# Kernel optimization log

Measured on AMD Instinct MI355X. Metric: run time of the kernel, lower is better.

The kernel has to match this reference:

```python
import jax, jax.numpy as jnp
import numpy as np

OBS, HID, H, A = 128, 256, 512, 16
T, B = 256, 256


def setup_inputs() -> dict:
    key = jax.random.key(0)
    ks = jax.random.split(key, 8)
    s = lambda k, shape, fan_in: jax.random.normal(k, shape, jnp.float32) / np.sqrt(fan_in).astype(np.float32)
    return {
        "x": jax.random.normal(ks[0], (T, B, OBS), jnp.float32),
        "W_enc": s(ks[1], (OBS, HID), OBS),
        "b_enc": jnp.zeros((HID,), jnp.float32),
        "Wi": s(ks[2], (HID, 4 * H), HID),      # input->gates kernel (i,f,g,o)
        "Wh": s(ks[3], (H, 4 * H), H),          # hidden->gates kernel
        "b_lstm": jnp.zeros((4 * H,), jnp.float32),
        "W_mu": s(ks[4], (H, A), H),
        "b_mu": jnp.zeros((A,), jnp.float32),
        "log_std": jnp.zeros((1, A), jnp.float32),
        "W_v": s(ks[5], (H, 1), H),
        "b_v": jnp.zeros((1,), jnp.float32),
    }


def reference(x, W_enc, b_enc, Wi, Wh, b_lstm, W_mu, b_mu, log_std, W_v, b_v):
    # Encoder MLP: Linear + gelu, mapping obs_dim -> hidden_features.
    feats = jax.nn.gelu(x @ W_enc + b_enc)            # (T, B, HID)
    # Precompute the input contribution to all 4 gates for every timestep
    # (same math as flax OptimizedLSTMCell, hoisted out of the scan).
    x_gates = feats @ Wi + b_lstm                      # (T, B, 4H)
    bsz = x.shape[1]
    c0 = jnp.zeros((bsz, H), x.dtype)
    h0 = jnp.zeros((bsz, H), x.dtype)

    def step(carry, xg):
        c, h = carry
        z = xg + h @ Wh                                # (B, 4H)
        i, f, g, o = jnp.split(z, 4, axis=-1)          # flax gate order i,f,g,o
        c_new = jax.nn.sigmoid(f) * c + jax.nn.sigmoid(i) * jnp.tanh(g)
        h_new = jax.nn.sigmoid(o) * jnp.tanh(c_new)
        return (c_new, h_new), h_new

    _, hs = jax.lax.scan(step, (c0, h0), x_gates)      # hs: (T, B, H)
    # Heads (dropout is identity in eval/deterministic mode).
    mu = hs @ W_mu + b_mu                              # (T, B, A)
    sigma = jnp.broadcast_to(jnp.exp(log_std), mu.shape)
    value = hs @ W_v + b_v                             # (T, B, 1)
    return mu, sigma, value
```

## Files before the change

kernel.cpp:

```cpp
#include <hip/hip_runtime.h>
#include <stdint.h>

#define T_STEPS 256
#define BATCH   256
#define OBS     128
#define HID     256
#define HSZ     512
#define NG      16
#define RPG     16
#define NSLICES 16
#define HCS     32
#define GCOLS   128
#define RING_SLOT_W 65536

typedef __attribute__((ext_vector_type(8))) short short8;
typedef __attribute__((ext_vector_type(4))) float f32x4;
typedef __attribute__((ext_vector_type(4))) int   i32x4;

__device__ __forceinline__ unsigned short f2bf(float x) {
    union { float f; uint32_t u; } v; v.f = x;
    uint32_t r = v.u + 0x7FFF + ((v.u >> 16) & 1);
    return (unsigned short)(r >> 16);
}
__device__ __forceinline__ float sigmoidf_(float x) { return 1.f / (1.f + __expf(-x)); }
__device__ __forceinline__ float tanhf_(float x)    { return 1.f - 2.f / (1.f + __expf(2.f * x)); }

#define GLD4(d0, d1, d2, d3, p, O0, O1, O2, O3)                                 \
    asm volatile("global_load_dwordx4 %0, %4, off offset:" #O0 " sc0 sc1\n\t"   \
                 "global_load_dwordx4 %1, %4, off offset:" #O1 " sc0 sc1\n\t"   \
                 "global_load_dwordx4 %2, %4, off offset:" #O2 " sc0 sc1\n\t"   \
                 "global_load_dwordx4 %3, %4, off offset:" #O3 " sc0 sc1"       \
                 : "=&v"(d0), "=&v"(d1), "=&v"(d2), "=&v"(d3) : "v"(p))

__global__ __launch_bounds__(256) void enc_kernel(
    const float* __restrict__ x, const float* __restrict__ W_enc,
    const float* __restrict__ b_enc, unsigned short* __restrict__ feats) {
    __shared__ unsigned short wlds[HID * OBS];
    int tid = threadIdx.x;
    for (int idx = tid; idx < OBS * HID; idx += 256) {
        int k = idx >> 8, n = idx & 255;
        int byte = ((n * OBS + k) * 2) ^ ((n & 7) << 4);
        *(unsigned short*)((char*)wlds + byte) = f2bf(W_enc[k * HID + n]);
    }
    __syncthreads();
    int wave = tid >> 6, lane = tid & 63;
    long m0 = (long)blockIdx.x * 64 + wave * 16;
    int arow = lane & 15, kq = lane >> 4;
    f32x4 acc[16];
    f32x4 z4 = {0.f, 0.f, 0.f, 0.f};
#pragma unroll
    for (int i = 0; i < 16; i++) acc[i] = z4;
#pragma unroll
    for (int kk = 0; kk < OBS; kk += 32) {
        const float* ap = x + (m0 + arow) * OBS + kk + kq * 8;
        float4 a0 = *(const float4*)ap;
        float4 a1 = *(const float4*)(ap + 4);
        short8 af;
        af[0] = (short)f2bf(a0.x); af[1] = (short)f2bf(a0.y);
        af[2] = (short)f2bf(a0.z); af[3] = (short)f2bf(a0.w);
        af[4] = (short)f2bf(a1.x); af[5] = (short)f2bf(a1.y);
        af[6] = (short)f2bf(a1.z); af[7] = (short)f2bf(a1.w);
#pragma unroll
        for (int nt = 0; nt < 16; nt++) {
            int n = nt * 16 + arow;
            int byte = ((n * OBS + kk + kq * 8) * 2) ^ ((n & 7) << 4);
            short8 bf = *(const short8*)((char*)wlds + byte);
            acc[nt] = __builtin_amdgcn_mfma_f32_16x16x32_bf16(af, bf, acc[nt], 0, 0, 0);
        }
    }
#pragma unroll
    for (int nt = 0; nt < 16; nt++) {
        int col = nt * 16 + (lane & 15);
        float bias = b_enc[col];
#pragma unroll
        for (int j = 0; j < 4; j++) {
            long row = m0 + kq * 4 + j;
            float z = acc[nt][j] + bias;
            float zc = 0.79788456f * (z + 0.044715f * z * z * z);
            float g = 0.5f * z * (1.f + tanhf_(zc));
            feats[row * HID + col] = f2bf(g);
        }
    }
}

__global__ __launch_bounds__(256) void prep_wi(
    const float* __restrict__ Wi, unsigned short* __restrict__ Wipk) {
    int t = blockIdx.x * 256 + threadIdx.x;
    int f = t & 15, l = (t >> 4) & 63, w = (t >> 10) & 3, s = t >> 12;
    int ct = f >> 3, i = f & 7;
    int n = w * 32 + ct * 16 + (l & 15);
    int colg = (n & 3) * HSZ + s * HCS + (n >> 2);
    int kbase = i * 32 + (l >> 4) * 8;
    short8 v;
#pragma unroll
    for (int j = 0; j < 8; j++) v[j] = (short)f2bf(Wi[(kbase + j) * 2048 + colg]);
    *(short8*)(Wipk + (long)t * 8) = v;
}

__device__ __forceinline__ void spin_flags(const uint32_t* fl, int lane) {
    const uint32_t* p = fl + (lane & 15);
    while (true) {
        uint32_t got = (lane < 16)
            ? __hip_atomic_load(p, __ATOMIC_RELAXED, __HIP_MEMORY_SCOPE_AGENT) : 1u;
        if (__all(got != 0)) break;
    }
}

__global__ __launch_bounds__(256) void scan_kernel(
    const float* __restrict__ Wh, const float* __restrict__ b_lstm,
    const unsigned short* __restrict__ feats, const unsigned short* __restrict__ Wipk,
    uint32_t* __restrict__ ring, uint32_t* __restrict__ flags,
    uint32_t* __restrict__ hs32) {
    __shared__ unsigned short whs[GCOLS * HSZ];
    __shared__ unsigned short hst[RPG * HSZ];
    __shared__ float zt[RPG][132];
    const int tid = threadIdx.x;
    const int g = blockIdx.x & 15;
    const int slice = blockIdx.x >> 4;
    const int rowg = g * RPG;

    for (int idx = tid; idx < GCOLS * HSZ; idx += 256) {
        int n = idx & 127, k = idx >> 7;
        int colg = (n & 3) * HSZ + slice * HCS + (n >> 2);
        int byte = ((n * HSZ + k) * 2) ^ ((n & 7) << 4);
        *(unsigned short*)((char*)whs + byte) = f2bf(Wh[k * 2048 + colg]);
    }
    const int wave = tid >> 6, lane = tid & 63;
    const int wc = wave * 32;
    const int arow = lane & 15, kq = lane >> 4;
    const int n0 = wc + arow, n1 = wc + 16 + arow;
    short8 wif0[8], wif1[8];
    {
        const short8* wp = (const short8*)Wipk + ((slice * 4 + wave) * 64 + lane) * 16;
#pragma unroll
        for (int i = 0; i < 8; i++) { wif0[i] = wp[i]; wif1[i] = wp[8 + i]; }
    }
    const int grow = tid >> 4, hp = tid & 15;
    float bl0[4], bl1[4];
#pragma unroll
    for (int q = 0; q < 4; q++) {
        bl0[q] = b_lstm[q * HSZ + slice * HCS + 2 * hp];
        bl1[q] = b_lstm[q * HSZ + slice * HCS + 2 * hp + 1];
    }
    float c0 = 0.f, c1 = 0.f;
    const int srow = tid >> 4, sc64 = tid & 15;
    const int sw = (srow & 7) << 4;
    f32x4 z4 = {0.f, 0.f, 0.f, 0.f};
    __syncthreads();

    for (int t = 0; t < T_STEPS; ++t) {
        f32x4 acc0 = z4, acc1 = z4;
        const char* fb = (const char*)feats + ((long)t * BATCH + rowg + arow) * (HID * 2) + kq * 16;
#pragma unroll
        for (int i = 0; i < 8; i++) {
            short8 af = *(const short8*)(fb + i * 64);
            acc0 = __builtin_amdgcn_mfma_f32_16x16x32_bf16(af, wif0[i], acc0, 0, 0, 0);
            acc1 = __builtin_amdgcn_mfma_f32_16x16x32_bf16(af, wif1[i], acc1, 0, 0, 0);
        }
        __builtin_amdgcn_sched_barrier(0);
        if (t > 0) {
            if (tid < 64) spin_flags(flags + ((long)g * T_STEPS + t - 1) * 16, lane);
            __syncthreads();
            const char* hb = (const char*)ring + ((t - 1) & 3) * (RING_SLOT_W * 4)
                           + (rowg + srow) * 1024 + sc64 * 64;
            i32x4 S0, S1, S2, S3;
            GLD4(S0, S1, S2, S3, hb, 0, 16, 32, 48);
            asm volatile("s_waitcnt vmcnt(0)" ::: "memory");
            __builtin_amdgcn_sched_barrier(0);
            int sb = srow * 1024 + sc64 * 64;
            *(i32x4*)((char*)hst + ((sb +  0) ^ sw)) = S0;
            *(i32x4*)((char*)hst + ((sb + 16) ^ sw)) = S1;
            *(i32x4*)((char*)hst + ((sb + 32) ^ sw)) = S2;
            *(i32x4*)((char*)hst + ((sb + 48) ^ sw)) = S3;
            __syncthreads();
#pragma unroll
            for (int i = 0; i < 16; i++) {
                short8 ah = *(const short8*)((char*)hst
                              + ((arow * 1024 + i * 64 + kq * 16) ^ ((arow & 7) << 4)));
                int kk = i * 32 + kq * 8;
                short8 b0 = *(const short8*)((char*)whs + (((n0 * HSZ + kk) * 2) ^ ((n0 & 7) << 4)));
                short8 b1 = *(const short8*)((char*)whs + (((n1 * HSZ + kk) * 2) ^ ((n1 & 7) << 4)));
                acc0 = __builtin_amdgcn_mfma_f32_16x16x32_bf16(ah, b0, acc0, 0, 0, 0);
                acc1 = __builtin_amdgcn_mfma_f32_16x16x32_bf16(ah, b1, acc1, 0, 0, 0);
            }
        }
#pragma unroll
        for (int j = 0; j < 4; j++) {
            zt[kq * 4 + j][wc + arow]      = acc0[j];
            zt[kq * 4 + j][wc + 16 + arow] = acc1[j];
        }
        __syncthreads();
        float4 r0 = *(const float4*)&zt[grow][8 * hp];
        float4 r1 = *(const float4*)&zt[grow][8 * hp + 4];
        c0 = sigmoidf_(r0.y + bl0[1]) * c0 + sigmoidf_(r0.x + bl0[0]) * tanhf_(r0.z + bl0[2]);
        c1 = sigmoidf_(r1.y + bl1[1]) * c1 + sigmoidf_(r1.x + bl1[0]) * tanhf_(r1.z + bl1[2]);
        float h0 = sigmoidf_(r0.w + bl0[3]) * tanhf_(c0);
        float h1 = sigmoidf_(r1.w + bl1[3]) * tanhf_(c1);
        uint32_t wv = (uint32_t)f2bf(h0) | ((uint32_t)f2bf(h1) << 16);
        uint32_t* wp = ring + (t & 3) * RING_SLOT_W + (rowg + grow) * 256 + slice * 16 + hp;
        __hip_atomic_store(wp, wv, __ATOMIC_RELAXED, __HIP_MEMORY_SCOPE_AGENT);
        hs32[((long)t * BATCH + rowg + grow) * 256 + slice * 16 + hp] = wv;
        __syncthreads();
        if (tid == 0)
            __hip_atomic_store(flags + ((long)g * T_STEPS + t) * 16 + slice, 1u,
                               __ATOMIC_RELAXED, __HIP_MEMORY_SCOPE_AGENT);
    }
}

__global__ __launch_bounds__(256) void heads_kernel(
    const unsigned short* __restrict__ hs, const float* __restrict__ W_mu,
    const float* __restrict__ b_mu, const float* __restrict__ log_std,
    const float* __restrict__ W_v, const float* __restrict__ b_v,
    float* __restrict__ mu_out, float* __restrict__ sig_out,
    float* __restrict__ val_out) {
    __shared__ unsigned short wlds[32 * HSZ];
    int tid = threadIdx.x;
    for (int idx = tid; idx < 32 * HSZ; idx += 256) {
        int n = idx & 31, k = idx >> 5;
        float w = 0.f;
        if (n < 16) w = W_mu[k * 16 + n];
        else if (n == 16) w = W_v[k];
        int byte = ((n * HSZ + k) * 2) ^ ((n & 7) << 4);
        *(unsigned short*)((char*)wlds + byte) = f2bf(w);
    }
    __syncthreads();
    int wave = tid >> 6, lane = tid & 63;
    long m0 = (long)blockIdx.x * 64 + wave * 16;
    int arow = lane & 15, kq = lane >> 4;
    f32x4 acc0 = {0.f, 0.f, 0.f, 0.f}, acc1 = {0.f, 0.f, 0.f, 0.f};
    const unsigned short* hr = hs + (m0 + arow) * HSZ + kq * 8;
#pragma unroll
    for (int kk = 0; kk < HSZ; kk += 32) {
        short8 af = *(const short8*)(hr + kk);
        int n0 = arow;
        int b0 = ((n0 * HSZ + kk + kq * 8) * 2) ^ ((n0 & 7) << 4);
        short8 bf0 = *(const short8*)((char*)wlds + b0);
        acc0 = __builtin_amdgcn_mfma_f32_16x16x32_bf16(af, bf0, acc0, 0, 0, 0);
        int n1 = 16 + arow;
        int b1 = ((n1 * HSZ + kk + kq * 8) * 2) ^ ((n1 & 7) << 4);
        short8 bf1 = *(const short8*)((char*)wlds + b1);
        acc1 = __builtin_amdgcn_mfma_f32_16x16x32_bf16(af, bf1, acc1, 0, 0, 0);
    }
    int col = lane & 15;
    float bm = b_mu[col];
    float sg = __expf(log_std[col]);
#pragma unroll
    for (int j = 0; j < 4; j++) {
        long row = m0 + kq * 4 + j;
        mu_out[row * 16 + col]  = acc0[j] + bm;
        sig_out[row * 16 + col] = sg;
    }
    if (col == 0) {
        float bv = b_v[0];
#pragma unroll
        for (int j = 0; j < 4; j++) {
            long row = m0 + kq * 4 + j;
            val_out[row] = acc1[j] + bv;
        }
    }
}

extern "C" void kernel_launch(void* const* d_in, const int* in_sizes, int n_in,
                              void* d_out, int out_size, void* d_ws, size_t ws_size,
                              hipStream_t stream) {
    const float* x      = (const float*)d_in[0];
    const float* W_enc  = (const float*)d_in[1];
    const float* b_enc  = (const float*)d_in[2];
    const float* Wi     = (const float*)d_in[3];
    const float* Wh     = (const float*)d_in[4];
    const float* b_lstm = (const float*)d_in[5];
    const float* W_mu   = (const float*)d_in[6];
    const float* b_mu   = (const float*)d_in[7];
    const float* lstd   = (const float*)d_in[8];
    const float* W_v    = (const float*)d_in[9];
    const float* b_v    = (const float*)d_in[10];

    char* ws = (char*)d_ws;
    uint32_t*       flags = (uint32_t*)ws;
    uint32_t*       ring  = (uint32_t*)(ws + (512 << 10));
    unsigned short* Wipk  = (unsigned short*)(ws + (1536 << 10));
    unsigned short* feats = (unsigned short*)(ws + (3584 << 10));
    unsigned short* hs    = (unsigned short*)(ws + (3584 << 10) + 33554432);

    float* mu_out  = (float*)d_out;
    float* sig_out = mu_out + 1048576;
    float* val_out = mu_out + 2097152;

    hipMemsetAsync(flags, 0, NG * T_STEPS * NSLICES * sizeof(uint32_t), stream);
    prep_wi<<<dim3(256), dim3(256), 0, stream>>>(Wi, Wipk);
    enc_kernel<<<dim3(1024), dim3(256), 0, stream>>>(x, W_enc, b_enc, feats);
    scan_kernel<<<dim3(256), dim3(256), 0, stream>>>(Wh, b_lstm, feats, Wipk,
                                                     ring, flags, (uint32_t*)hs);
    heads_kernel<<<dim3(1024), dim3(256), 0, stream>>>(hs, W_mu, b_mu, lstd, W_v, b_v,
                                                       mu_out, sig_out, val_out);
}
```

Baseline: 1.020 ms.

## Replace flag-based step sync with sentinel-polled ring and register-resident gate reshuffle

Drops the per-step flag array and block-wide barriers. Consumers poll the h ring data directly until no 0xFFFFFFFF sentinel is left, and producers reset the slot from two steps back to the sentinel. Half of the Wh slice now lives in registers, prepacked by a new prep_wh kernel, while the other half stays in LDS. The hidden-state tile is double-buffered, the feats rows for the next step are prefetched, and the gate reshuffle uses lane shuffles in place of an LDS transpose. Together these remove two syncthreads and a flag round-trip per timestep from the serial critical path. The cost is higher register pressure and reliance on the sentinel never being a legitimate pair of bf16 values.

Result: slower. 1.451 ms (+42.2%).

```diff
diff --git a/kernel.cpp b/kernel.cpp
--- a/kernel.cpp
+++ b/kernel.cpp
@@ -10,7 +10,6 @@
 #define RPG     16
 #define NSLICES 16
 #define HCS     32
-#define GCOLS   128
 #define RING_SLOT_W 65536
 
 typedef __attribute__((ext_vector_type(8))) short short8;
@@ -97,113 +96,160 @@
     *(short8*)(Wipk + (long)t * 8) = v;
 }
 
-__device__ __forceinline__ void spin_flags(const uint32_t* fl, int lane) {
-    const uint32_t* p = fl + (lane & 15);
-    while (true) {
-        uint32_t got = (lane < 16)
-            ? __hip_atomic_load(p, __ATOMIC_RELAXED, __HIP_MEMORY_SCOPE_AGENT) : 1u;
-        if (__all(got != 0)) break;
-    }
-}
-
-__global__ __launch_bounds__(256) void scan_kernel(
-    const float* __restrict__ Wh, const float* __restrict__ b_lstm,
-    const unsigned short* __restrict__ feats, const unsigned short* __restrict__ Wipk,
-    uint32_t* __restrict__ ring, uint32_t* __restrict__ flags,
+__global__ __launch_bounds__(256) void prep_wh(
+    const float* __restrict__ Wh, unsigned short* __restrict__ Whpk) {
+    int t = blockIdx.x * 256 + threadIdx.x;
+    int l = t & 63, i = (t >> 6) & 15, w = (t >> 10) & 3, s = t >> 12;
+    int n = w * 32 + (l & 15);
+    int colg = (n & 3) * HSZ + s * HCS + (n >> 2);
+    int kbase = i * 32 + (l >> 4) * 8;
+    short8 v;
+#pragma unroll
+    for (int j = 0; j < 8; j++) v[j] = (short)f2bf(Wh[(kbase + j) * 2048 + colg]);
+    *(short8*)(Whpk + (long)t * 8) = v;
+}
+
+__global__ __launch_bounds__(256, 1) void scan_kernel(
+    const float* __restrict__ b_lstm, const unsigned short* __restrict__ feats,
+    const unsigned short* __restrict__ Wipk, const unsigned short* __restrict__ Whpk,
+    const float* __restrict__ Wh, uint32_t* __restrict__ ring,
     uint32_t* __restrict__ hs32) {
-    __shared__ unsigned short whs[GCOLS * HSZ];
-    __shared__ unsigned short hst[RPG * HSZ];
-    __shared__ float zt[RPG][132];
+    __shared__ unsigned short whs[64 * HSZ];
+    __shared__ unsigned short hst[2 * RPG * HSZ];
     const int tid = threadIdx.x;
     const int g = blockIdx.x & 15;
     const int slice = blockIdx.x >> 4;
     const int rowg = g * RPG;
-
-    for (int idx = tid; idx < GCOLS * HSZ; idx += 256) {
-        int n = idx & 127, k = idx >> 7;
-        int colg = (n & 3) * HSZ + slice * HCS + (n >> 2);
-        int byte = ((n * HSZ + k) * 2) ^ ((n & 7) << 4);
+    const int wave = tid >> 6, lane = tid & 63;
+    const int arow = lane & 15, kq = lane >> 4;
+
+    for (int idx = tid; idx < 64 * HSZ; idx += 256) {
+        int np = idx & 63, k = idx >> 6;
+        int n1 = (np >> 4) * 32 + 16 + (np & 15);
+        int colg = (n1 & 3) * HSZ + slice * HCS + (n1 >> 2);
+        int byte = ((np * HSZ + k) * 2) ^ ((np & 7) << 4);
         *(unsigned short*)((char*)whs + byte) = f2bf(Wh[k * 2048 + colg]);
     }
-    const int wave = tid >> 6, lane = tid & 63;
-    const int wc = wave * 32;
-    const int arow = lane & 15, kq = lane >> 4;
-    const int n0 = wc + arow, n1 = wc + 16 + arow;
-    short8 wif0[8], wif1[8];
+    short8 wif0[8], wif1[8], whb[16];
     {
         const short8* wp = (const short8*)Wipk + ((slice * 4 + wave) * 64 + lane) * 16;
 #pragma unroll
         for (int i = 0; i < 8; i++) { wif0[i] = wp[i]; wif1[i] = wp[8 + i]; }
-    }
-    const int grow = tid >> 4, hp = tid & 15;
+        const short8* hp8 = (const short8*)Whpk;
+#pragma unroll
+        for (int i = 0; i < 16; i++)
+            whb[i] = hp8[((slice * 4 + wave) * 16 + i) * 64 + lane];
+    }
+    const int a_ = arow >> 2;
+    const int hcol0 = slice * HCS + wave * 8 + a_;
     float bl0[4], bl1[4];
 #pragma unroll
     for (int q = 0; q < 4; q++) {
-        bl0[q] = b_lstm[q * HSZ + slice * HCS + 2 * hp];
-        bl1[q] = b_lstm[q * HSZ + slice * HCS + 2 * hp + 1];
-    }
+        bl0[q] = b_lstm[q * HSZ + hcol0];
+        bl1[q] = b_lstm[q * HSZ + hcol0 + 4];
+    }
+    const int row = kq * 4 + (arow & 3);
+    int colw = slice * 16 + wave * 4 + ((a_ & 1) ? 2 + (a_ >> 1) : (a_ >> 1));
     float c0 = 0.f, c1 = 0.f;
     const int srow = tid >> 4, sc64 = tid & 15;
     const int sw = (srow & 7) << 4;
+    short8 ff[8];
+    {
+        const char* fb = (const char*)feats + ((long)(rowg + arow)) * (HID * 2) + kq * 16;
+#pragma unroll
+        for (int i = 0; i < 8; i++) ff[i] = *(const short8*)(fb + i * 64);
+    }
     f32x4 z4 = {0.f, 0.f, 0.f, 0.f};
     __syncthreads();
 
     for (int t = 0; t < T_STEPS; ++t) {
         f32x4 acc0 = z4, acc1 = z4;
-        const char* fb = (const char*)feats + ((long)t * BATCH + rowg + arow) * (HID * 2) + kq * 16;
 #pragma unroll
         for (int i = 0; i < 8; i++) {
-            short8 af = *(const short8*)(fb + i * 64);
-            acc0 = __builtin_amdgcn_mfma_f32_16x16x32_bf16(af, wif0[i], acc0, 0, 0, 0);
-            acc1 = __builtin_amdgcn_mfma_f32_16x16x32_bf16(af, wif1[i], acc1, 0, 0, 0);
+            acc0 = __builtin_amdgcn_mfma_f32_16x16x32_bf16(ff[i], wif0[i], acc0, 0, 0, 0);
+            acc1 = __builtin_amdgcn_mfma_f32_16x16x32_bf16(ff[i], wif1[i], acc1, 0, 0, 0);
+        }
+        {
+            int tn = (t + 1 < T_STEPS) ? t + 1 : t;
+            const char* fb = (const char*)feats
+                           + ((long)tn * BATCH + rowg + arow) * (HID * 2) + kq * 16;
+#pragma unroll
+            for (int i = 0; i < 8; i++) ff[i] = *(const short8*)(fb + i * 64);
         }
         __builtin_amdgcn_sched_barrier(0);
         if (t > 0) {
-            if (tid < 64) spin_flags(flags + ((long)g * T_STEPS + t - 1) * 16, lane);
-            __syncthreads();
-            const char* hb = (const char*)ring + ((t - 1) & 3) * (RING_SLOT_W * 4)
+            const char* pb = (const char*)ring + ((t - 1) & 3) * (RING_SLOT_W * 4)
                            + (rowg + srow) * 1024 + sc64 * 64;
             i32x4 S0, S1, S2, S3;
-            GLD4(S0, S1, S2, S3, hb, 0, 16, 32, 48);
-            asm volatile("s_waitcnt vmcnt(0)" ::: "memory");
+            while (true) {
+                GLD4(S0, S1, S2, S3, pb, 0, 16, 32, 48);
+                asm volatile("s_waitcnt vmcnt(0)" ::: "memory");
+                bool ok = S0[0] != -1 && S0[1] != -1 && S0[2] != -1 && S0[3] != -1
+                       && S1[0] != -1 && S1[1] != -1 && S1[2] != -1 && S1[3] != -1
+                       && S2[0] != -1 && S2[1] != -1 && S2[2] != -1 && S2[3] != -1
+                       && S3[0] != -1 && S3[1] != -1 && S3[2] != -1 && S3[3] != -1;
+                if (ok) break;
+                __builtin_amdgcn_s_sleep(1);
+            }
             __builtin_amdgcn_sched_barrier(0);
+            char* hb = (char*)hst + (t & 1) * 16384;
             int sb = srow * 1024 + sc64 * 64;
-            *(i32x4*)((char*)hst + ((sb +  0) ^ sw)) = S0;
-            *(i32x4*)((char*)hst + ((sb + 16) ^ sw)) = S1;
-            *(i32x4*)((char*)hst + ((sb + 32) ^ sw)) = S2;
-            *(i32x4*)((char*)hst + ((sb + 48) ^ sw)) = S3;
-            __syncthreads();
+            *(i32x4*)(hb + ((sb +  0) ^ sw)) = S0;
+            *(i32x4*)(hb + ((sb + 16) ^ sw)) = S1;
+            *(i32x4*)(hb + ((sb + 32) ^ sw)) = S2;
+            *(i32x4*)(hb + ((sb + 48) ^ sw)) = S3;
+        }
+        __syncthreads();
+        if (t > 0) {
+            const char* hb = (const char*)hst + (t & 1) * 16384;
+            const int np = wave * 16 + arow;
 #pragma unroll
             for (int i = 0; i < 16; i++) {
-                short8 ah = *(const short8*)((char*)hst
+                short8 ah = *(const short8*)(hb
                               + ((arow * 1024 + i * 64 + kq * 16) ^ ((arow & 7) << 4)));
-                int kk = i * 32 + kq * 8;
-                short8 b0 = *(const short8*)((char*)whs + (((n0 * HSZ + kk) * 2) ^ ((n0 & 7) << 4)));
-                short8 b1 = *(const short8*)((char*)whs + (((n1 * HSZ + kk) * 2) ^ ((n1 & 7) << 4)));
-                acc0 = __builtin_amdgcn_mfma_f32_16x16x32_bf16(ah, b0, acc0, 0, 0, 0);
+                short8 b1 = *(const short8*)((char*)whs
+                              + ((np * 1024 + i * 64 + kq * 16) ^ ((np & 7) << 4)));
+                acc0 = __builtin_amdgcn_mfma_f32_16x16x32_bf16(ah, whb[i], acc0, 0, 0, 0);
                 acc1 = __builtin_amdgcn_mfma_f32_16x16x32_bf16(ah, b1, acc1, 0, 0, 0);
             }
         }
-#pragma unroll
-        for (int j = 0; j < 4; j++) {
-            zt[kq * 4 + j][wc + arow]      = acc0[j];
-            zt[kq * 4 + j][wc + 16 + arow] = acc1[j];
-        }
-        __syncthreads();
-        float4 r0 = *(const float4*)&zt[grow][8 * hp];
-        float4 r1 = *(const float4*)&zt[grow][8 * hp + 4];
-        c0 = sigmoidf_(r0.y + bl0[1]) * c0 + sigmoidf_(r0.x + bl0[0]) * tanhf_(r0.z + bl0[2]);
-        c1 = sigmoidf_(r1.y + bl1[1]) * c1 + sigmoidf_(r1.x + bl1[0]) * tanhf_(r1.z + bl1[2]);
-        float h0 = sigmoidf_(r0.w + bl0[3]) * tanhf_(c0);
-        float h1 = sigmoidf_(r1.w + bl1[3]) * tanhf_(c1);
-        uint32_t wv = (uint32_t)f2bf(h0) | ((uint32_t)f2bf(h1) << 16);
-        uint32_t* wp = ring + (t & 3) * RING_SLOT_W + (rowg + grow) * 256 + slice * 16 + hp;
-        __hip_atomic_store(wp, wv, __ATOMIC_RELAXED, __HIP_MEMORY_SCOPE_AGENT);
-        hs32[((long)t * BATCH + rowg + grow) * 256 + slice * 16 + hp] = wv;
-        __syncthreads();
-        if (tid == 0)
-            __hip_atomic_store(flags + ((long)g * T_STEPS + t) * 16 + slice, 1u,
-                               __ATOMIC_RELAXED, __HIP_MEMORY_SCOPE_AGENT);
+        float C0, C1, C2, C3, D0, D1, D2, D3;
+        {
+            float s0 = __shfl_xor(acc0[0], 1), s1 = __shfl_xor(acc0[1], 1);
+            float s2 = __shfl_xor(acc0[2], 1), s3 = __shfl_xor(acc0[3], 1);
+            bool o1 = arow & 1;
+            float b0_ = o1 ? s1 : acc0[0], b1_ = o1 ? acc0[1] : s0;
+            float b2_ = o1 ? s3 : acc0[2], b3_ = o1 ? acc0[3] : s2;
+            float r0 = __shfl_xor(b0_, 2), r1 = __shfl_xor(b1_, 2);
+            float r2 = __shfl_xor(b2_, 2), r3 = __shfl_xor(b3_, 2);
+            bool o2 = arow & 2;
+            C0 = o2 ? r2 : b0_; C1 = o2 ? r3 : b1_;
+            C2 = o2 ? b2_ : r0; C3 = o2 ? b3_ : r1;
+            s0 = __shfl_xor(acc1[0], 1); s1 = __shfl_xor(acc1[1], 1);
+            s2 = __shfl_xor(acc1[2], 1); s3 = __shfl_xor(acc1[3], 1);
+            b0_ = o1 ? s1 : acc1[0]; b1_ = o1 ? acc1[1] : s0;
+            b2_ = o1 ? s3 : acc1[2]; b3_ = o1 ? acc1[3] : s2;
+            r0 = __shfl_xor(b0_, 2); r1 = __shfl_xor(b1_, 2);
+            r2 = __shfl_xor(b2_, 2); r3 = __shfl_xor(b3_, 2);
+            D0 = o2 ? r2 : b0_; D1 = o2 ? r3 : b1_;
+            D2 = o2 ? b2_ : r0; D3 = o2 ? b3_ : r1;
+        }
+        c0 = sigmoidf_(C1 + bl0[1]) * c0 + sigmoidf_(C0 + bl0[0]) * tanhf_(C2 + bl0[2]);
+        c1 = sigmoidf_(D1 + bl1[1]) * c1 + sigmoidf_(D0 + bl1[0]) * tanhf_(D2 + bl1[2]);
+        float h0 = sigmoidf_(C3 + bl0[3]) * tanhf_(c0);
+        float h1 = sigmoidf_(D3 + bl1[3]) * tanhf_(c1);
+        uint32_t hu0 = f2bf(h0), hu1 = f2bf(h1);
+        uint32_t p0 = (uint32_t)__shfl_xor((int)hu0, 4);
+        uint32_t p1 = (uint32_t)__shfl_xor((int)hu1, 4);
+        uint32_t word = (a_ & 1) ? (p1 | (hu1 << 16)) : (hu0 | (p0 << 16));
+        uint32_t* wp = ring + (t & 3) * RING_SLOT_W + (rowg + row) * 256 + colw;
+        asm volatile("global_store_dword %0, %1, off sc0 sc1" :: "v"(wp), "v"(word) : "memory");
+        hs32[((long)t * BATCH + rowg + row) * 256 + colw] = word;
+        if (t >= 2) {
+            uint32_t* rp = ring + ((t - 2) & 3) * RING_SLOT_W + (rowg + row) * 256 + colw;
+            uint32_t sen = 0xFFFFFFFFu;
+            asm volatile("global_store_dword %0, %1, off sc0 sc1" :: "v"(rp), "v"(sen) : "memory");
+        }
     }
 }
 
@@ -276,21 +322,22 @@
     const float* b_v    = (const float*)d_in[10];
 
     char* ws = (char*)d_ws;
-    uint32_t*       flags = (uint32_t*)ws;
-    uint32_t*       ring  = (uint32_t*)(ws + (512 << 10));
-    unsigned short* Wipk  = (unsigned short*)(ws + (1536 << 10));
-    unsigned short* feats = (unsigned short*)(ws + (3584 << 10));
-    unsigned short* hs    = (unsigned short*)(ws + (3584 << 10) + 33554432);
+    uint32_t*       ring  = (uint32_t*)ws;
+    unsigned short* Wipk  = (unsigned short*)(ws + (1 << 20));
+    unsigned short* Whpk  = (unsigned short*)(ws + (2 << 20));
+    unsigned short* feats = (unsigned short*)(ws + (3 << 20));
+    unsigned short* hs    = (unsigned short*)(ws + (3 << 20) + 33554432);
 
     float* mu_out  = (float*)d_out;
     float* sig_out = mu_out + 1048576;
     float* val_out = mu_out + 2097152;
 
-    hipMemsetAsync(flags, 0, NG * T_STEPS * NSLICES * sizeof(uint32_t), stream);
+    hipMemsetAsync(ring, 0xFF, 4 * RING_SLOT_W * sizeof(uint32_t), stream);
     prep_wi<<<dim3(256), dim3(256), 0, stream>>>(Wi, Wipk);
+    prep_wh<<<dim3(256), dim3(256), 0, stream>>>(Wh, Whpk);
     enc_kernel<<<dim3(1024), dim3(256), 0, stream>>>(x, W_enc, b_enc, feats);
-    scan_kernel<<<dim3(256), dim3(256), 0, stream>>>(Wh, b_lstm, feats, Wipk,
-                                                     ring, flags, (uint32_t*)hs);
+    scan_kernel<<<dim3(256), dim3(256), 0, stream>>>(b_lstm, feats, Wipk, Whpk, Wh,
+                                                     ring, (uint32_t*)hs);
     heads_kernel<<<dim3(1024), dim3(256), 0, stream>>>(hs, W_mu, b_mu, lstd, W_v, b_v,
                                                        mu_out, sig_out, val_out);
 }
```
